# Performance work log

Measured on AMD Instinct MI355X. Metric: run time of the kernel, lower is better.

Reference implementation:

```python
import jax, jax.numpy as jnp
import numpy as np

B, T, D, H = 4, 2048, 1024, 16
HD = D // H  # 64

def setup_inputs() -> dict:
    key = jax.random.key(0)
    k1, k2, k3 = jax.random.split(key, 3)
    scale = 1.0 / np.sqrt(D)
    x = jax.random.normal(k1, (B, T, D), dtype=jnp.float32)
    w_qkv = jax.random.normal(k2, (D, 3 * D), dtype=jnp.float32) * scale
    w_o = jax.random.normal(k3, (D, D), dtype=jnp.float32) * scale
    return {"x": x, "w_qkv": w_qkv, "w_o": w_o}

def reference(x, w_qkv, w_o):
    b, t, d = x.shape
    qkv = jnp.einsum('btd,de->bte', x, w_qkv)  # [B,T,3D]
    q, k, v = jnp.split(qkv, 3, axis=-1)
    # [B,H,T,hd]
    q = q.reshape(b, t, H, HD).transpose(0, 2, 1, 3)
    k = k.reshape(b, t, H, HD).transpose(0, 2, 1, 3)
    v = v.reshape(b, t, H, HD).transpose(0, 2, 1, 3)
    scores = jnp.einsum('bhqd,bhkd->bhqk', q, k) * (1.0 / jnp.sqrt(jnp.asarray(HD, x.dtype)))
    causal = jnp.tril(jnp.ones((t, t), dtype=bool))
    scores = jnp.where(causal[None, None, :, :], scores, -jnp.inf)
    weights = jax.nn.softmax(scores, axis=-1)
    out = jnp.einsum('bhqk,bhkd->bhqd', weights, v)
    out = out.transpose(0, 2, 1, 3).reshape(b, t, d)
    return jnp.einsum('btd,de->bte', out, w_o)
```

## Files before the change

kernel.cpp:

```cpp
#include <hip/hip_runtime.h>
#include <hip/hip_bf16.h>
#include <stdint.h>

#define HD 64
#define NH 16
#define TT 2048
#define DD 1024

typedef uint16_t u16;
typedef __bf16 bf16_t;
typedef bf16_t bf16x8 __attribute__((ext_vector_type(8)));
typedef float f32x4 __attribute__((ext_vector_type(4)));

__device__ __forceinline__ u16 f2b(float f) {
    union { float f; uint32_t u; } v; v.f = f;
    uint32_t u = v.u;
    u += 0x7fff + ((u >> 16) & 1);
    return (u16)(u >> 16);
}

__device__ __forceinline__ u16 b16(float f) {
    union { __bf16 h; u16 u; } c; c.h = (__bf16)f; return c.u;
}

__device__ __forceinline__ void gload16(const void* g, void* l) {
    __builtin_amdgcn_global_load_lds(
        (__attribute__((address_space(1))) void*)g,
        (__attribute__((address_space(3))) void*)l, 16, 0, 0);
}


__global__ void f32_to_bf16_vec(const float* __restrict__ in, u16* __restrict__ out, int n4) {
    int i = blockIdx.x * 256 + threadIdx.x;
    if (i >= n4) return;
    float4 v = ((const float4*)in)[i];
    ushort4 r;
    r.x = f2b(v.x); r.y = f2b(v.y); r.z = f2b(v.z); r.w = f2b(v.w);
    ((ushort4*)out)[i] = r;
}

__global__ void transpose_f32_bf16(const float* __restrict__ in, u16* __restrict__ out, int R, int C) {
    __shared__ float tile[32][33];
    const int tx = threadIdx.x, ty = threadIdx.y;
    const int c0 = blockIdx.x * 32, r0 = blockIdx.y * 32;
#pragma unroll
    for (int j = 0; j < 32; j += 8)
        tile[ty + j][tx] = in[(size_t)(r0 + ty + j) * C + c0 + tx];
    __syncthreads();
#pragma unroll
    for (int j = 0; j < 32; j += 8)
        out[(size_t)(c0 + ty + j) * R + r0 + tx] = f2b(tile[tx][ty + j]);
}


template<int MODE>
__global__ __launch_bounds__(256, 2)
void gemm_bt(const u16* __restrict__ A, const u16* __restrict__ Bt,
             int M, int N, int K,
             u16* __restrict__ oq, u16* __restrict__ ok, u16* __restrict__ ovT,
             float* __restrict__ of)
{
    __shared__ __align__(16) u16 As[128 * 32];
    __shared__ __align__(16) u16 Bs[128 * 32];
    const int tid = threadIdx.x;
    const int lane = tid & 63, l15 = lane & 15, g = lane >> 4;
    const int wv = tid >> 6, wr = wv >> 1, wc = wv & 1;
    const long row0 = (long)blockIdx.y * 128;
    const long col0 = (long)blockIdx.x * 128;

    const int cA = tid, cB = tid + 256;
    const u16* a0 = A + (row0 + (cA >> 2)) * K + (cA & 3) * 8;
    const u16* a1 = A + (row0 + (cB >> 2)) * K + (cB & 3) * 8;
    const u16* b0 = Bt + (col0 + (cA >> 2)) * K + (cA & 3) * 8;
    const u16* b1 = Bt + (col0 + (cB >> 2)) * K + (cB & 3) * 8;

    const f32x4 z4 = {0.f, 0.f, 0.f, 0.f};
    f32x4 acc[4][4];
#pragma unroll
    for (int i = 0; i < 4; i++)
#pragma unroll
        for (int n = 0; n < 4; n++) acc[i][n] = z4;

    for (int k0 = 0; k0 < K; k0 += 32) {
        gload16(a0 + k0, &As[cA * 8]);
        gload16(a1 + k0, &As[cB * 8]);
        gload16(b0 + k0, &Bs[cA * 8]);
        gload16(b1 + k0, &Bs[cB * 8]);
        __syncthreads();
        bf16x8 af[4], bfr[4];
#pragma unroll
        for (int i = 0; i < 4; i++) af[i]  = *(const bf16x8*)&As[(wr * 64 + i * 16 + l15) * 32 + g * 8];
#pragma unroll
        for (int n = 0; n < 4; n++) bfr[n] = *(const bf16x8*)&Bs[(wc * 64 + n * 16 + l15) * 32 + g * 8];
#pragma unroll
        for (int i = 0; i < 4; i++)
#pragma unroll
            for (int n = 0; n < 4; n++)
                acc[i][n] = __builtin_amdgcn_mfma_f32_16x16x32_bf16(af[i], bfr[n], acc[i][n], 0, 0, 0);
        __syncthreads();
    }

    if (MODE == 0) {
        const int which = (int)(col0 >> 10);
        const long b = row0 >> 11;
#pragma unroll
        for (int i = 0; i < 4; i++) {
            const long r = row0 + wr * 64 + i * 16 + g * 4;
            const long t = r & (TT - 1);
#pragma unroll
            for (int n = 0; n < 4; n++) {
                const long c = col0 + wc * 64 + n * 16 + l15;
                const int h  = (int)((c >> 6) & 15);
                const int hd = (int)(c & 63);
                if (which == 0) {
#pragma unroll
                    for (int e = 0; e < 4; e++)
                        oq[((b * NH + h) * TT + t + e) * HD + hd] = f2b(acc[i][n][e] * 0.125f);
                } else if (which == 1) {
#pragma unroll
                    for (int e = 0; e < 4; e++)
                        ok[((b * NH + h) * TT + t + e) * HD + hd] = f2b(acc[i][n][e]);
                } else {
                    ushort4 pk;
                    pk.x = f2b(acc[i][n][0]); pk.y = f2b(acc[i][n][1]);
                    pk.z = f2b(acc[i][n][2]); pk.w = f2b(acc[i][n][3]);
                    *(ushort4*)&ovT[((b * NH + h) * HD + hd) * TT + t] = pk;
                }
            }
        }
    } else {
#pragma unroll
        for (int i = 0; i < 4; i++) {
            const long r = row0 + wr * 64 + i * 16 + g * 4;
#pragma unroll
            for (int n = 0; n < 4; n++) {
                const long c = col0 + wc * 64 + n * 16 + l15;
#pragma unroll
                for (int e = 0; e < 4; e++)
                    of[(r + e) * (long)N + c] = acc[i][n][e];
            }
        }
    }
}


__global__ __launch_bounds__(256, 3)
void attn_fwd(const u16* __restrict__ gq, const u16* __restrict__ gk,
              const u16* __restrict__ gvT, u16* __restrict__ o)
{
    __shared__ __align__(16) u16 Klds[2][64 * 64];
    __shared__ __align__(16) u16 Vlds[2][64 * 64];
    __shared__ __align__(16) u16 Plds[4][32 * 64];

    const int tid = threadIdx.x;
    const int wv = tid >> 6, lane = tid & 63, l15 = lane & 15, g = lane >> 4;
    const int bh = blockIdx.x & 63;
    const int qt = 15 - (blockIdx.x >> 6);
    const int q0 = qt * 128;
    const int qw0 = q0 + wv * 32;

    const u16* qbase = gq + (size_t)bh * TT * HD;
    const u16* kbase = gk + (size_t)bh * TT * HD;
    const u16* vbase = gvT + (size_t)bh * HD * TT;

    const float NEG_INF = -__builtin_inff();
    const f32x4 z4 = {0.f, 0.f, 0.f, 0.f};

    bf16x8 qf[2][2];
#pragma unroll
    for (int qi = 0; qi < 2; qi++)
#pragma unroll
        for (int hs = 0; hs < 2; hs++)
            qf[qi][hs] = *(const bf16x8*)(qbase + (size_t)(qw0 + qi * 16 + l15) * HD + hs * 32 + g * 8);

    f32x4 o_acc[2][4];
    float m[2], ls[2];
#pragma unroll
    for (int qi = 0; qi < 2; qi++) {
#pragma unroll
        for (int n = 0; n < 4; n++) o_acc[qi][n] = z4;
        m[qi] = NEG_INF; ls[qi] = 0.f;
    }

    const int r0_ = tid >> 3, c0_ = tid & 7;
    const int r1_ = (tid + 256) >> 3, c1_ = (tid + 256) & 7;

#define STAGE(buf, k0s)                                                                    \
    do {                                                                                   \
        gload16(kbase + (size_t)((k0s) + r0_) * HD + ((c0_ ^ (r0_ & 7)) * 8), &Klds[buf][tid * 8]);          \
        gload16(kbase + (size_t)((k0s) + r1_) * HD + ((c1_ ^ (r1_ & 7)) * 8), &Klds[buf][(tid + 256) * 8]);  \
        gload16(vbase + (size_t)r0_ * TT + (k0s) + ((c0_ ^ (r0_ & 7)) * 8), &Vlds[buf][tid * 8]);            \
        gload16(vbase + (size_t)r1_ * TT + (k0s) + ((c1_ ^ (r1_ & 7)) * 8), &Vlds[buf][(tid + 256) * 8]);    \
    } while (0)

    const int nkt = q0 / 64 + 2;
    STAGE(0, 0);
    for (int kt = 0; kt < nkt; ++kt) {
        const int k0 = kt * 64;
        const int cur = kt & 1;
        if (kt + 1 < nkt) {
            STAGE(cur ^ 1, k0 + 64);
            asm volatile("s_waitcnt vmcnt(4)" ::: "memory");
        } else {
            asm volatile("s_waitcnt vmcnt(0)" ::: "memory");
        }
        __builtin_amdgcn_s_barrier();
        if (k0 <= qw0 + 31) {
            const int sw = l15 & 7;
            f32x4 s2[2][4];
            __builtin_amdgcn_s_setprio(1);
#pragma unroll
            for (int kb = 0; kb < 4; kb++) {
                bf16x8 kf0 = *(const bf16x8*)&Klds[cur][(kb * 16 + l15) * 64 + ((g ^ sw) * 8)];
                bf16x8 kf1 = *(const bf16x8*)&Klds[cur][(kb * 16 + l15) * 64 + (((4 + g) ^ sw) * 8)];
#pragma unroll
                for (int qi = 0; qi < 2; qi++) {
                    f32x4 t0 = __builtin_amdgcn_mfma_f32_16x16x32_bf16(kf0, qf[qi][0], z4, 0, 0, 0);
                    s2[qi][kb] = __builtin_amdgcn_mfma_f32_16x16x32_bf16(kf1, qf[qi][1], t0, 0, 0, 0);
                }
            }
            __builtin_amdgcn_s_setprio(0);
            if (k0 + 63 > qw0) {
#pragma unroll
                for (int qi = 0; qi < 2; qi++)
#pragma unroll
                    for (int kb = 0; kb < 4; kb++)
#pragma unroll
                        for (int e = 0; e < 4; e++) {
                            const int kk = k0 + kb * 16 + g * 4 + e;
                            const int qq = qw0 + qi * 16 + l15;
                            if (kk > qq) s2[qi][kb][e] = NEG_INF;
                        }
            }
#pragma unroll
            for (int qi = 0; qi < 2; qi++) {
                f32x4 mx = s2[qi][0];
#pragma unroll
                for (int kb = 1; kb < 4; kb++)
#pragma unroll
                    for (int e = 0; e < 4; e++) mx[e] = fmaxf(mx[e], s2[qi][kb][e]);
                float pmax = fmaxf(fmaxf(mx[0], mx[1]), fmaxf(mx[2], mx[3]));
                pmax = fmaxf(pmax, __shfl_xor(pmax, 16));
                pmax = fmaxf(pmax, __shfl_xor(pmax, 32));
                float mn = m[qi];
                const int resc = !__all(pmax <= mn + 8.f);
                if (resc) {
                    const float mold = mn;
                    mn = fmaxf(mold, pmax);
                    m[qi] = mn;
                    const float sc = __expf(mold - mn);
                    ls[qi] *= sc;
#pragma unroll
                    for (int e = 0; e < 4; e++) {
                        const float sce = __shfl(sc, (lane & 48) + (((lane >> 4) & 3) << 2) + e);
#pragma unroll
                        for (int n = 0; n < 4; n++) o_acc[qi][n][e] *= sce;
                    }
                }
                const int prow = qi * 16 + l15;
                u16* pb = &Plds[wv][prow * 64];
                float rsum = 0.f;
#pragma unroll
                for (int kb = 0; kb < 4; kb++) {
                    const float p0 = __expf(s2[qi][kb][0] - mn);
                    const float p1 = __expf(s2[qi][kb][1] - mn);
                    const float p2 = __expf(s2[qi][kb][2] - mn);
                    const float p3 = __expf(s2[qi][kb][3] - mn);
                    rsum += (p0 + p1) + (p2 + p3);
                    ushort4 pk;
                    pk.x = b16(p0); pk.y = b16(p1); pk.z = b16(p2); pk.w = b16(p3);
                    *(ushort4*)&pb[(((kb << 2) + g) ^ l15) * 4] = pk;
                }
                rsum += __shfl_xor(rsum, 16);
                rsum += __shfl_xor(rsum, 32);
                ls[qi] += rsum;
            }
#pragma unroll
            for (int ks = 0; ks < 2; ks++) {
                bf16x8 vf[4];
#pragma unroll
                for (int n = 0; n < 4; n++)
                    vf[n] = *(const bf16x8*)&Vlds[cur][(n * 16 + l15) * 64 + (((ks * 4 + g) ^ sw) * 8)];
                __builtin_amdgcn_s_setprio(1);
#pragma unroll
                for (int qi = 0; qi < 2; qi++) {
                    const u16* pb = &Plds[wv][(qi * 16 + l15) * 64];
                    const int G0 = ((ks << 3) + (g << 1)) ^ l15;
                    const int G1 = ((ks << 3) + (g << 1) + 1) ^ l15;
                    const uint2 ra = *(const uint2*)&pb[G0 * 4];
                    const uint2 rb = *(const uint2*)&pb[G1 * 4];
                    union { uint32_t w[4]; bf16x8 v; } pu;
                    pu.w[0] = ra.x; pu.w[1] = ra.y; pu.w[2] = rb.x; pu.w[3] = rb.y;
#pragma unroll
                    for (int n = 0; n < 4; n++)
                        o_acc[qi][n] = __builtin_amdgcn_mfma_f32_16x16x32_bf16(pu.v, vf[n], o_acc[qi][n], 0, 0, 0);
                }
                __builtin_amdgcn_s_setprio(0);
            }
        }
        __builtin_amdgcn_s_barrier();
    }
#undef STAGE

    const int b = bh >> 4, h = bh & 15;
#pragma unroll
    for (int qi = 0; qi < 2; qi++) {
        const float linv = 1.f / ls[qi];
#pragma unroll
        for (int e = 0; e < 4; e++) {
            const float inv = __shfl(linv, (lane & 48) + (((lane >> 4) & 3) << 2) + e);
            const int t = qw0 + qi * 16 + g * 4 + e;
#pragma unroll
            for (int n = 0; n < 4; n++)
                o[((size_t)(b * TT + t)) * DD + h * HD + n * 16 + l15] = f2b(o_acc[qi][n][e] * inv);
        }
    }
}


extern "C" void kernel_launch(void* const* d_in, const int* in_sizes, int n_in,
                              void* d_out, int out_size, void* d_ws, size_t ws_size,
                              hipStream_t stream)
{
    const float* x     = (const float*)d_in[0];
    const float* w_qkv = (const float*)d_in[1];
    const float* w_o   = (const float*)d_in[2];
    float* out = (float*)d_out;
    char* ws = (char*)d_ws;

    u16* xb    = (u16*)(ws);
    u16* wqkvT = (u16*)(ws + 16777216);
    u16* woT   = (u16*)(ws + 23068672);
    u16* wsq   = (u16*)(ws + 25165824);
    u16* wsk   = (u16*)(ws + 41943040);
    u16* wsvT  = (u16*)(ws + 58720256);
    u16* attno = (u16*)(ws + 75497472);

    f32_to_bf16_vec<<<8192, 256, 0, stream>>>(x, xb, 2097152);
    dim3 tb(32, 8);
    transpose_f32_bf16<<<dim3(96, 32), tb, 0, stream>>>(w_qkv, wqkvT, 1024, 3072);
    transpose_f32_bf16<<<dim3(32, 32), tb, 0, stream>>>(w_o,   woT,   1024, 1024);

    gemm_bt<0><<<dim3(24, 64), 256, 0, stream>>>(xb, wqkvT, 8192, 3072, 1024, wsq, wsk, wsvT, nullptr);
    attn_fwd<<<1024, 256, 0, stream>>>(wsq, wsk, wsvT, attno);
    gemm_bt<1><<<dim3(8, 64), 256, 0, stream>>>(attno, woT, 8192, 1024, 1024, nullptr, nullptr, nullptr, out);
}
```

Measured before the change: 175.3 us.

## Double-buffer GEMM LDS tiles with swizzled layout and prefetch pipelining

The projection GEMM now keeps two LDS buffers and issues the next K-slice's direct-to-LDS loads before computing on the current one, waiting with explicit vmcnt counts instead of a full sync. The global source column chunk is XOR-swizzled so the fragment reads from LDS hit fewer bank conflicts. It also raises the occupancy hint to 3 blocks per CU and bumps wave priority around the MFMA block. The cost is double the LDS per block, which may cap occupancy, and correctness depends on the swizzle on the load side matching the one on the read side.

Measured after the change: 174.0 us. No clear change (-0.7%).

```diff
diff --git a/kernel.cpp b/kernel.cpp
--- a/kernel.cpp
+++ b/kernel.cpp
@@ -54,14 +54,14 @@
 
 
 template<int MODE>
-__global__ __launch_bounds__(256, 2)
+__global__ __launch_bounds__(256, 3)
 void gemm_bt(const u16* __restrict__ A, const u16* __restrict__ Bt,
              int M, int N, int K,
              u16* __restrict__ oq, u16* __restrict__ ok, u16* __restrict__ ovT,
              float* __restrict__ of)
 {
-    __shared__ __align__(16) u16 As[128 * 32];
-    __shared__ __align__(16) u16 Bs[128 * 32];
+    __shared__ __align__(16) u16 As[2][128 * 32];
+    __shared__ __align__(16) u16 Bs[2][128 * 32];
     const int tid = threadIdx.x;
     const int lane = tid & 63, l15 = lane & 15, g = lane >> 4;
     const int wv = tid >> 6, wr = wv >> 1, wc = wv & 1;
@@ -69,10 +69,10 @@
     const long col0 = (long)blockIdx.x * 128;
 
     const int cA = tid, cB = tid + 256;
-    const u16* a0 = A + (row0 + (cA >> 2)) * K + (cA & 3) * 8;
-    const u16* a1 = A + (row0 + (cB >> 2)) * K + (cB & 3) * 8;
-    const u16* b0 = Bt + (col0 + (cA >> 2)) * K + (cA & 3) * 8;
-    const u16* b1 = Bt + (col0 + (cB >> 2)) * K + (cB & 3) * 8;
+    const u16* a0 = A + (row0 + (cA >> 2)) * K + (((cA & 3) ^ ((cA >> 3) & 3)) * 8);
+    const u16* a1 = A + (row0 + (cB >> 2)) * K + (((cB & 3) ^ ((cB >> 3) & 3)) * 8);
+    const u16* b0 = Bt + (col0 + (cA >> 2)) * K + (((cA & 3) ^ ((cA >> 3) & 3)) * 8);
+    const u16* b1 = Bt + (col0 + (cB >> 2)) * K + (((cB & 3) ^ ((cB >> 3) & 3)) * 8);
 
     const f32x4 z4 = {0.f, 0.f, 0.f, 0.f};
     f32x4 acc[4][4];
@@ -81,24 +81,44 @@
 #pragma unroll
         for (int n = 0; n < 4; n++) acc[i][n] = z4;
 
-    for (int k0 = 0; k0 < K; k0 += 32) {
-        gload16(a0 + k0, &As[cA * 8]);
-        gload16(a1 + k0, &As[cB * 8]);
-        gload16(b0 + k0, &Bs[cA * 8]);
-        gload16(b1 + k0, &Bs[cB * 8]);
-        __syncthreads();
+    const int swz = (l15 >> 1) & 3;
+
+#define GSTAGE(buf, k0s)                          \
+    do {                                          \
+        gload16(a0 + (k0s), &As[buf][cA * 8]);    \
+        gload16(a1 + (k0s), &As[buf][cB * 8]);    \
+        gload16(b0 + (k0s), &Bs[buf][cA * 8]);    \
+        gload16(b1 + (k0s), &Bs[buf][cB * 8]);    \
+    } while (0)
+
+    const int niter = K >> 5;
+    GSTAGE(0, 0);
+    for (int it = 0; it < niter; ++it) {
+        const int cur = it & 1;
+        if (it + 1 < niter) {
+            GSTAGE(cur ^ 1, (it + 1) * 32);
+            asm volatile("s_waitcnt vmcnt(4)" ::: "memory");
+        } else {
+            asm volatile("s_waitcnt vmcnt(0)" ::: "memory");
+        }
+        __builtin_amdgcn_s_barrier();
         bf16x8 af[4], bfr[4];
 #pragma unroll
-        for (int i = 0; i < 4; i++) af[i]  = *(const bf16x8*)&As[(wr * 64 + i * 16 + l15) * 32 + g * 8];
-#pragma unroll
-        for (int n = 0; n < 4; n++) bfr[n] = *(const bf16x8*)&Bs[(wc * 64 + n * 16 + l15) * 32 + g * 8];
+        for (int i = 0; i < 4; i++)
+            af[i]  = *(const bf16x8*)&As[cur][(wr * 64 + i * 16 + l15) * 32 + ((g ^ swz) << 3)];
+#pragma unroll
+        for (int n = 0; n < 4; n++)
+            bfr[n] = *(const bf16x8*)&Bs[cur][(wc * 64 + n * 16 + l15) * 32 + ((g ^ swz) << 3)];
+        __builtin_amdgcn_s_setprio(1);
 #pragma unroll
         for (int i = 0; i < 4; i++)
 #pragma unroll
             for (int n = 0; n < 4; n++)
                 acc[i][n] = __builtin_amdgcn_mfma_f32_16x16x32_bf16(af[i], bfr[n], acc[i][n], 0, 0, 0);
-        __syncthreads();
-    }
+        __builtin_amdgcn_s_setprio(0);
+        __builtin_amdgcn_s_barrier();
+    }
+#undef GSTAGE
 
     if (MODE == 0) {
         const int which = (int)(col0 >> 10);
```

## Rewrite projection GEMMs with 128x256 tiles, triple-buffered LDS, swizzle, XCD remap

Applied to the files above, without the earlier changes.

The two projection GEMMs now use 512-thread blocks computing 128x256 tiles with a K-step of 64. Global-to-LDS loads are triple-buffered and tracked with explicit vmcnt waits so the next tiles load while MFMAs run. LDS columns are XOR-swizzled to avoid bank conflicts, and workgroup IDs are remapped across the 8 XCDs for better L2 locality. The block count drops and LDS use rises to about 144KB per block, which may limit occupancy and leave CUs idle on the smaller output GEMM.

Result: slower. 179.3 us (+2.3%).

```diff
diff --git a/kernel.cpp b/kernel.cpp
--- a/kernel.cpp
+++ b/kernel.cpp
@@ -54,25 +54,28 @@
 
 
 template<int MODE>
-__global__ __launch_bounds__(256, 2)
-void gemm_bt(const u16* __restrict__ A, const u16* __restrict__ Bt,
-             int M, int N, int K,
+__global__ __launch_bounds__(512, 2)
+void gemm256(const u16* __restrict__ A, const u16* __restrict__ Bt,
+             int N, int K,
              u16* __restrict__ oq, u16* __restrict__ ok, u16* __restrict__ ovT,
              float* __restrict__ of)
 {
-    __shared__ __align__(16) u16 As[128 * 32];
-    __shared__ __align__(16) u16 Bs[128 * 32];
+    __shared__ __align__(16) u16 As[3][128 * 64];
+    __shared__ __align__(16) u16 Bs[3][256 * 64];
     const int tid = threadIdx.x;
     const int lane = tid & 63, l15 = lane & 15, g = lane >> 4;
-    const int wv = tid >> 6, wr = wv >> 1, wc = wv & 1;
-    const long row0 = (long)blockIdx.y * 128;
-    const long col0 = (long)blockIdx.x * 128;
-
-    const int cA = tid, cB = tid + 256;
-    const u16* a0 = A + (row0 + (cA >> 2)) * K + (cA & 3) * 8;
-    const u16* a1 = A + (row0 + (cB >> 2)) * K + (cB & 3) * 8;
-    const u16* b0 = Bt + (col0 + (cA >> 2)) * K + (cA & 3) * 8;
-    const u16* b1 = Bt + (col0 + (cB >> 2)) * K + (cB & 3) * 8;
+    const int wid = tid >> 6, wm = wid >> 2, wn = wid & 3;
+
+    const int gx = gridDim.x;
+    const int nwg = gx * gridDim.y;
+    const int wgid = blockIdx.y * gx + blockIdx.x;
+    const int cpx = nwg >> 3;
+    const int sid = (wgid & 7) * cpx + (wgid >> 3);
+    const long row0 = (long)(sid / gx) * 128;
+    const long col0 = (long)(sid % gx) * 256;
+
+    const u16* Ag = A + row0 * K;
+    const u16* Bg = Bt + col0 * K;
 
     const f32x4 z4 = {0.f, 0.f, 0.f, 0.f};
     f32x4 acc[4][4];
@@ -81,63 +84,103 @@
 #pragma unroll
         for (int n = 0; n < 4; n++) acc[i][n] = z4;
 
-    for (int k0 = 0; k0 < K; k0 += 32) {
-        gload16(a0 + k0, &As[cA * 8]);
-        gload16(a1 + k0, &As[cB * 8]);
-        gload16(b0 + k0, &Bs[cA * 8]);
-        gload16(b1 + k0, &Bs[cB * 8]);
-        __syncthreads();
-        bf16x8 af[4], bfr[4];
-#pragma unroll
-        for (int i = 0; i < 4; i++) af[i]  = *(const bf16x8*)&As[(wr * 64 + i * 16 + l15) * 32 + g * 8];
-#pragma unroll
-        for (int n = 0; n < 4; n++) bfr[n] = *(const bf16x8*)&Bs[(wc * 64 + n * 16 + l15) * 32 + g * 8];
-#pragma unroll
-        for (int i = 0; i < 4; i++)
+    const int swz = l15 & 7;
+
+#define STG(t_, s_) do {                                                                                    \
+        const int ko = (t_) << 6;                                                                           \
+        { const int c = tid;        const int r_ = c >> 3;                                                  \
+          gload16(Ag + (size_t)r_ * K + ko + (((c & 7) ^ (r_ & 7)) << 3), &As[s_][c << 3]); }               \
+        { const int c = tid + 512;  const int r_ = c >> 3;                                                  \
+          gload16(Ag + (size_t)r_ * K + ko + (((c & 7) ^ (r_ & 7)) << 3), &As[s_][c << 3]); }               \
+        { const int c = tid;        const int r_ = c >> 3;                                                  \
+          gload16(Bg + (size_t)r_ * K + ko + (((c & 7) ^ (r_ & 7)) << 3), &Bs[s_][c << 3]); }               \
+        { const int c = tid + 512;  const int r_ = c >> 3;                                                  \
+          gload16(Bg + (size_t)r_ * K + ko + (((c & 7) ^ (r_ & 7)) << 3), &Bs[s_][c << 3]); }               \
+        { const int c = tid + 1024; const int r_ = c >> 3;                                                  \
+          gload16(Bg + (size_t)r_ * K + ko + (((c & 7) ^ (r_ & 7)) << 3), &Bs[s_][c << 3]); }               \
+        { const int c = tid + 1536; const int r_ = c >> 3;                                                  \
+          gload16(Bg + (size_t)r_ * K + ko + (((c & 7) ^ (r_ & 7)) << 3), &Bs[s_][c << 3]); }               \
+    } while (0)
+
+    const int NT = K >> 6;
+    STG(0, 0);
+    STG(1, 1);
+    int scur = 0;
+    for (int t = 0; t < NT; ++t) {
+        if (t + 1 < NT) asm volatile("s_waitcnt vmcnt(6)" ::: "memory");
+        else            asm volatile("s_waitcnt vmcnt(0)" ::: "memory");
+        __builtin_amdgcn_s_barrier();
+        const int sstg = (scur == 0) ? 2 : scur - 1;
+        if (t + 2 < NT) STG(t + 2, sstg);
+
+        bf16x8 a0[4], b0[4], a1[4], b1[4];
+        const int p0 = (g ^ swz) << 3, p1 = ((g ^ swz) ^ 4) << 3;
+#pragma unroll
+        for (int m = 0; m < 4; m++) {
+            const int rA = (wm * 64 + m * 16 + l15) * 64;
+            a0[m] = *(const bf16x8*)&As[scur][rA + p0];
+            a1[m] = *(const bf16x8*)&As[scur][rA + p1];
+        }
+#pragma unroll
+        for (int n = 0; n < 4; n++) {
+            const int rB = (wn * 64 + n * 16 + l15) * 64;
+            b0[n] = *(const bf16x8*)&Bs[scur][rB + p0];
+            b1[n] = *(const bf16x8*)&Bs[scur][rB + p1];
+        }
+        __builtin_amdgcn_s_setprio(1);
+#pragma unroll
+        for (int m = 0; m < 4; m++)
 #pragma unroll
             for (int n = 0; n < 4; n++)
-                acc[i][n] = __builtin_amdgcn_mfma_f32_16x16x32_bf16(af[i], bfr[n], acc[i][n], 0, 0, 0);
-        __syncthreads();
-    }
+                acc[m][n] = __builtin_amdgcn_mfma_f32_16x16x32_bf16(a0[m], b0[n], acc[m][n], 0, 0, 0);
+#pragma unroll
+        for (int m = 0; m < 4; m++)
+#pragma unroll
+            for (int n = 0; n < 4; n++)
+                acc[m][n] = __builtin_amdgcn_mfma_f32_16x16x32_bf16(a1[m], b1[n], acc[m][n], 0, 0, 0);
+        __builtin_amdgcn_s_setprio(0);
+        scur = (scur == 2) ? 0 : scur + 1;
+    }
+#undef STG
 
     if (MODE == 0) {
         const int which = (int)(col0 >> 10);
         const long b = row0 >> 11;
 #pragma unroll
-        for (int i = 0; i < 4; i++) {
-            const long r = row0 + wr * 64 + i * 16 + g * 4;
+        for (int m = 0; m < 4; m++) {
+            const long r = row0 + wm * 64 + m * 16 + g * 4;
             const long t = r & (TT - 1);
 #pragma unroll
             for (int n = 0; n < 4; n++) {
-                const long c = col0 + wc * 64 + n * 16 + l15;
+                const long c = col0 + wn * 64 + n * 16 + l15;
                 const int h  = (int)((c >> 6) & 15);
                 const int hd = (int)(c & 63);
                 if (which == 0) {
 #pragma unroll
                     for (int e = 0; e < 4; e++)
-                        oq[((b * NH + h) * TT + t + e) * HD + hd] = f2b(acc[i][n][e] * 0.125f);
+                        oq[((b * NH + h) * TT + t + e) * HD + hd] = f2b(acc[m][n][e] * 0.125f);
                 } else if (which == 1) {
 #pragma unroll
                     for (int e = 0; e < 4; e++)
-                        ok[((b * NH + h) * TT + t + e) * HD + hd] = f2b(acc[i][n][e]);
+                        ok[((b * NH + h) * TT + t + e) * HD + hd] = f2b(acc[m][n][e]);
                 } else {
                     ushort4 pk;
-                    pk.x = f2b(acc[i][n][0]); pk.y = f2b(acc[i][n][1]);
-                    pk.z = f2b(acc[i][n][2]); pk.w = f2b(acc[i][n][3]);
+                    pk.x = f2b(acc[m][n][0]); pk.y = f2b(acc[m][n][1]);
+                    pk.z = f2b(acc[m][n][2]); pk.w = f2b(acc[m][n][3]);
                     *(ushort4*)&ovT[((b * NH + h) * HD + hd) * TT + t] = pk;
                 }
             }
         }
     } else {
 #pragma unroll
-        for (int i = 0; i < 4; i++) {
-            const long r = row0 + wr * 64 + i * 16 + g * 4;
+        for (int m = 0; m < 4; m++) {
+            const long r = row0 + wm * 64 + m * 16 + g * 4;
 #pragma unroll
             for (int n = 0; n < 4; n++) {
-                const long c = col0 + wc * 64 + n * 16 + l15;
+                const long c = col0 + wn * 64 + n * 16 + l15;
 #pragma unroll
                 for (int e = 0; e < 4; e++)
-                    of[(r + e) * (long)N + c] = acc[i][n][e];
+                    of[(r + e) * (long)N + c] = acc[m][n][e];
             }
         }
     }
@@ -341,7 +384,7 @@
     transpose_f32_bf16<<<dim3(96, 32), tb, 0, stream>>>(w_qkv, wqkvT, 1024, 3072);
     transpose_f32_bf16<<<dim3(32, 32), tb, 0, stream>>>(w_o,   woT,   1024, 1024);
 
-    gemm_bt<0><<<dim3(24, 64), 256, 0, stream>>>(xb, wqkvT, 8192, 3072, 1024, wsq, wsk, wsvT, nullptr);
+    gemm256<0><<<dim3(12, 64), 512, 0, stream>>>(xb, wqkvT, 3072, 1024, wsq, wsk, wsvT, nullptr);
     attn_fwd<<<1024, 256, 0, stream>>>(wsq, wsk, wsvT, attno);
-    gemm_bt<1><<<dim3(8, 64), 256, 0, stream>>>(attno, woT, 8192, 1024, 1024, nullptr, nullptr, nullptr, out);
-}
+    gemm256<1><<<dim3(4, 64), 512, 0, stream>>>(attno, woT, 1024, 1024, nullptr, nullptr, nullptr, out);
+}
```
